# Kernel tuning notes

Hardware: AMD Instinct MI355X
Metric: run time of the kernel (lower is better)

Reference implementation:

```python
import jax, jax.numpy as jnp
import numpy as np

# ---- fixed architecture constants (hard-coded in Wavenet_Barebones.__init__) ----
B = 2
T_FRAMES = 64
UPS = (4, 4, 4, 4)
T = T_FRAMES * 256            # 16384 audio samples
VOCAB = 259
CH = 128
CC = 80                       # conditioning (mel) channels
K = 3                         # dilated conv kernel size
LAYERS = 24
LAYERS_PER_STACK = 6          # 24 // 4
FC1 = 512


def setup_inputs() -> dict:
    key = jax.random.key(0)
    ks = iter(jax.random.split(key, 32))
    nrm = lambda shape, s: jax.random.normal(next(ks), shape, jnp.float32) * s
    return {
        "x": jax.random.randint(next(ks), (B, T), 0, VOCAB),          # mu-law token ids
        "c": jax.random.normal(next(ks), (B, CC, T_FRAMES), jnp.float32),  # mel frames (B,C,Tf)
        "emb": nrm((VOCAB, CH), 1.0),
        "enc_w": nrm((CH, CH), 0.08), "enc_b": jnp.zeros((CH,), jnp.float32),
        "conv_w": nrm((LAYERS, CH, CH, K), 0.05),  # (L, out, in, k)
        "conv_b": jnp.zeros((LAYERS, CH), jnp.float32),
        "cond_w": nrm((LAYERS, CH, CC), 0.05),     # per-layer 1x1 local-conditioning proj
        "cond_b": jnp.zeros((LAYERS, CH), jnp.float32),
        "fc1_w": nrm((FC1, CH), 0.08), "fc1_b": jnp.zeros((FC1,), jnp.float32),
        "fc2_w": nrm((VOCAB, FC1), 0.04), "fc2_b": jnp.zeros((VOCAB,), jnp.float32),
        "ups_w": nrm((4, 3, 4), 0.3),              # 4 ConvTranspose2d kernels (freq=3, time=4)
        "ups_b": jnp.zeros((4,), jnp.float32),
    }


def _upsample(c, ups_w, ups_b):
    """r9y9 UpsampleNetwork: stack of ConvTranspose2d(1,1,(3,s),stride=(1,s),padding=(1,0)) + ReLU.
    c: (B, CC, Tf) -> (B, CC, Tf*256)."""
    y = c[:, None]  # (B, 1, CC, Tf)
    for i, s in enumerate(UPS):
        # transposed conv == input dilation by s + correlation with spatially-flipped kernel
        w = ups_w[i][::-1, ::-1][None, None]  # (O=1, I=1, 3, s)
        y = jax.lax.conv_general_dilated(
            y, w, window_strides=(1, 1),
            padding=[(1, 1), (s - 1, s - 1)],   # freq: kh-1-pad=1; time: kw-1-0=s-1
            lhs_dilation=(1, s),
            dimension_numbers=("NCHW", "OIHW", "NCHW"))
        y = jax.nn.relu(y + ups_b[i])
    return y[:, 0]  # (B, CC, T)


def reference(x, c, emb, enc_w, enc_b, conv_w, conv_b, cond_w, cond_b,
              fc1_w, fc1_b, fc2_w, fc2_b, ups_w, ups_b):
    # encode: embedding -> relu(linear)   (dropout is inference-disabled)
    h = jax.nn.relu(jnp.einsum("btc,oc->bto", emb[x], enc_w) + enc_b)  # (B,T,CH)
    cu = _upsample(c, ups_w, ups_b)                                     # (B,CC,T)
    h = h.transpose(0, 2, 1)                                            # (B,CH,T)
    dn = ("NCH", "OIH", "NCH")
    for l in range(LAYERS):
        d = 2 ** (l % LAYERS_PER_STACK)
        p = (K - 1) * d  # causal left pad
        y = jax.lax.conv_general_dilated(
            h, conv_w[l], window_strides=(1,), padding=[(p, 0)],
            rhs_dilation=(d,), dimension_numbers=dn)
        y = jax.nn.relu(y + conv_b[l][:, None])
        cond = jnp.einsum("oc,bct->bot", cond_w[l], cu) + cond_b[l][:, None]
        h = jax.nn.relu(y + cond + h)  # conditioning + residual, outer F.relu from forward loop
    h = h.transpose(0, 2, 1)                                            # (B,T,CH)
    h = jax.nn.relu(jnp.einsum("btc,oc->bto", h, fc1_w) + fc1_b)
    out = jnp.einsum("btf,of->bto", h, fc2_w) + fc2_b                   # (B,T,VOCAB)
    return out[:, :-1, :]
```

## Files before the change

### kernel.cpp

```cpp
#include <hip/hip_runtime.h>

typedef __bf16 bf16;
typedef __attribute__((ext_vector_type(8))) __bf16 bf16x8;
typedef __attribute__((ext_vector_type(4))) __bf16 bf16x4;
typedef __attribute__((ext_vector_type(4))) float f32x4;

namespace {
constexpr int Bn = 2;
constexpr int T  = 16384;
constexpr int NL = 24;
constexpr int VOC = 259;
}

#define MFMA_B16(a, b, c) __builtin_amdgcn_mfma_f32_16x16x32_bf16((a), (b), (c), 0, 0, 0)

__global__ void prep_wconv_k(const float* __restrict__ cw, const float* __restrict__ dw,
                             bf16* __restrict__ W2) {
  int total = NL * 61440;
  for (int idx = blockIdx.x * 256 + threadIdx.x; idx < total; idx += gridDim.x * 256) {
    int l = idx / 61440; int r = idx % 61440;
    int s = r >> 12; int of = (r >> 9) & 7; int lane = (r >> 3) & 63; int j = r & 7;
    int o = of * 16 + (lane & 15);
    int kk = (lane >> 4) * 8 + j;
    float v;
    if (s < 12) { int k = s >> 2; int c = (s & 3) * 32 + kk; v = cw[((l * 128 + o) * 128 + c) * 3 + k]; }
    else        { int cc = (s - 12) * 32 + kk; v = (cc < 80) ? dw[(l * 128 + o) * 80 + cc] : 0.f; }
    W2[idx] = (bf16)v;
  }
}

__global__ void prep_misc_k(const float* __restrict__ fc1w, const float* __restrict__ encw,
                            const float* __restrict__ emb, const float* __restrict__ fc2w,
                            bf16* __restrict__ fc1wb, bf16* __restrict__ encwb,
                            bf16* __restrict__ embb, bf16* __restrict__ w2f) {
  const int n1 = 65536, n2 = 16384, n3 = 33152, n4 = 196608;
  int total = n1 + n2 + n3 + n4;
  for (int idx = blockIdx.x * 256 + threadIdx.x; idx < total; idx += gridDim.x * 256) {
    if (idx < n1) { fc1wb[idx] = (bf16)fc1w[idx]; }
    else if (idx < n1 + n2) { int i = idx - n1; encwb[i] = (bf16)encw[i]; }
    else if (idx < n1 + n2 + n3) { int i = idx - n1 - n2; embb[i] = (bf16)emb[i]; }
    else {
      int r = idx - n1 - n2 - n3;
      int s = r / 12288; int r2 = r % 12288;
      int ot = r2 >> 9; int lane = (r2 >> 3) & 63; int j = r2 & 7;
      int o = ot * 16 + (lane & 15);
      int f = s * 32 + (lane >> 4) * 8 + j;
      w2f[r] = (bf16)((o < VOC) ? fc2w[o * 512 + f] : 0.f);
    }
  }
}

__global__ void ups_stage_k(const float* __restrict__ in, float* __restrict__ out,
                            const float* __restrict__ W, const float* __restrict__ bptr, int Win) {
  int Wout = Win * 4;
  int total = Bn * 80 * Wout;
  float bias = *bptr;
  for (int idx = blockIdx.x * 256 + threadIdx.x; idx < total; idx += gridDim.x * 256) {
    int w = idx % Wout; int rest = idx / Wout;
    int hrow = rest % 80; int b = rest / 80;
    int win = w >> 2; int kw = w & 3;
    float acc = bias;
#pragma unroll
    for (int kh = 0; kh < 3; ++kh) {
      int hr = hrow + 1 - kh;
      if (hr >= 0 && hr < 80) acc += in[(b * 80 + hr) * Win + win] * W[kh * 4 + kw];
    }
    out[idx] = fmaxf(acc, 0.f);
  }
}

__global__ void ups4_cuT_k(const float* __restrict__ in, const float* __restrict__ W,
                           const float* __restrict__ bptr, bf16* __restrict__ cuT2) {
  int total = Bn * 1024 * 3 * 512;
  float bias = *bptr;
  for (int idx = blockIdx.x * 256 + threadIdx.x; idx < total; idx += gridDim.x * 256) {
    int low = idx & 511; int j = low & 7; int lane = low >> 3;
    int g = idx >> 9; int sc = g % 3; int gt = g / 3; int tile = gt & 1023; int b = gt >> 10;
    int lr = lane & 15, lk = lane >> 4;
    int t = tile * 16 + lr;
    int cc = sc * 32 + lk * 8 + j;
    float v = 0.f;
    if (cc < 80) {
      int win = t >> 2, kw = t & 3;
      float acc = bias;
#pragma unroll
      for (int kh = 0; kh < 3; ++kh) {
        int hr = cc + 1 - kh;
        if (hr >= 0 && hr < 80) acc += in[(b * 80 + hr) * 4096 + win] * W[kh * 4 + kw];
      }
      v = fmaxf(acc, 0.f);
    }
    cuT2[idx] = (bf16)v;
  }
}

__global__ __launch_bounds__(256, 2) void encode_k(
    const int* __restrict__ x, const bf16* __restrict__ embb, const bf16* __restrict__ encwb,
    const float* __restrict__ encb, bf16* __restrict__ hbt) {
  __shared__ char Eb[16384];
  int t0 = blockIdx.x * 64, b = blockIdx.y;
  int tid = threadIdx.x, lane = tid & 63, wid = tid >> 6, wr = wid >> 1, wc = wid & 1;
  int lr = lane & 15, lk = lane >> 4;
  int tb = t0 + wc * 32;
  int xi[2];
#pragma unroll
  for (int n = 0; n < 2; ++n) xi[n] = x[b * T + tb + n * 16 + lr];
  f32x4 acc[4][2] = {};
#pragma unroll
  for (int s = 0; s < 4; ++s) {
    bf16x8 a[4], bb[2];
#pragma unroll
    for (int m = 0; m < 4; ++m) a[m] = *(const bf16x8*)(encwb + (wr * 64 + m * 16 + lr) * 128 + s * 32 + lk * 8);
#pragma unroll
    for (int n = 0; n < 2; ++n) bb[n] = *(const bf16x8*)(embb + xi[n] * 128 + s * 32 + lk * 8);
#pragma unroll
    for (int m = 0; m < 4; ++m)
#pragma unroll
      for (int n = 0; n < 2; ++n) acc[m][n] = MFMA_B16(a[m], bb[n], acc[m][n]);
  }
#pragma unroll
  for (int m = 0; m < 4; ++m)
#pragma unroll
    for (int n = 0; n < 2; ++n) {
      int obase = wr * 64 + m * 16 + lk * 4;
      int row = wc * 32 + n * 16 + lr;
      bf16x4 p;
#pragma unroll
      for (int r = 0; r < 4; ++r) p[r] = (bf16)fmaxf(acc[m][n][r] + encb[obase + r], 0.f);
      int byteo = obase * 2;
      int slot = ((byteo >> 4) ^ (row & 7)) & 15;
      *(bf16x4*)(Eb + row * 256 + (slot << 4) + (byteo & 15)) = p;
    }
  __syncthreads();
  const size_t btb = (size_t)b * T;
  for (int u = tid; u < 1024; u += 256) {
    int row = u >> 4, slot = u & 15;
    uint4 v = *(const uint4*)(Eb + row * 256 + ((((slot) ^ (row & 7)) & 15) << 4));
    *(uint4*)(hbt + (btb + t0 + row) * 128 + slot * 8) = v;
  }
}

template <int D1>
__global__ __launch_bounds__(512, 4) void layer2_k(
    const bf16* __restrict__ hbt_in, bf16* __restrict__ hbt_out,
    const bf16* __restrict__ W2, const bf16* __restrict__ cuT2,
    const float* __restrict__ cb1, const float* __restrict__ db1,
    const float* __restrict__ cb2, const float* __restrict__ db2) {
  constexpr int D2 = 2 * D1;
  constexpr int EXT = (D1 == 16) ? 64 : 16;
  constexpr int NMF = EXT / 16;
  constexpr int NF = NMF + 4;
  constexpr int NCH = (D1 == 16) ? 2 : 1;
  constexpr int NFC = NF / NCH;
  constexpr int AOFF = EXT + 2 * D1;
  constexpr int AR = 64 + AOFF;
  constexpr int BR = 64 + EXT;
  __shared__ uint4 Au[AR * 16];
  __shared__ uint4 Bu[BR * 16];
  char* AB = (char*)Au;
  char* BB = (char*)Bu;
  const int bx = blockIdx.x;
  const int tblk = ((bx & 7) << 5) | (bx >> 3);
  const int t0 = tblk * 64, b = blockIdx.y;
  const int tid = threadIdx.x, lane = tid & 63, wid = tid >> 6;
  const int lr = lane & 15, lk = lane >> 4;
  const size_t btb = (size_t)b * T;
  const size_t bt16 = (size_t)b * 1024;
  const bf16* Wa = W2;
  const bf16* Wb = W2 + 61440;

  uint4 zv; zv.x = zv.y = zv.z = zv.w = 0;
  for (int u = tid; u < AR * 16; u += 512) {
    int row = u >> 4, slot = u & 15;
    int t = t0 - AOFF + row;
    uint4 v = (t >= 0) ? *(const uint4*)(hbt_in + (btb + t) * 128 + slot * 8) : zv;
    *(uint4*)(AB + row * 256 + (((slot ^ (row & 7)) & 15) << 4)) = v;
  }
  __syncthreads();

  f32x4 hl[4];
  const int ob = wid * 16 + lk * 4;
  const f32x4 dv1 = *(const f32x4*)(db1 + ob);
  const int byteo = ob * 2, slot0 = byteo >> 4, wib = byteo & 15;
#pragma unroll
  for (int ch = 0; ch < NCH; ++ch) {
    const int fb = ch * NFC;
    f32x4 acc[NFC] = {};
#pragma unroll
    for (int s = 0; s < 12; ++s) {
      const int k = s >> 2, shift = (k - 2) * D1, sb = (s & 3) * 4;
      bf16x8 a = *(const bf16x8*)(Wa + ((s * 8 + wid) * 64 + lane) * 8);
#pragma unroll
      for (int n = 0; n < NFC; ++n) {
        int row = 2 * D1 + (fb + n) * 16 + lr + shift;
        int slot = ((sb + lk) ^ (row & 7)) & 15;
        bf16x8 bb = *(const bf16x8*)(AB + row * 256 + slot * 16);
        acc[n] = MFMA_B16(a, bb, acc[n]);
      }
    }
    {
      const f32x4 bv = *(const f32x4*)(cb1 + wid * 16 + lk * 4);
#pragma unroll
      for (int n = 0; n < NFC; ++n)
#pragma unroll
        for (int r = 0; r < 4; ++r) acc[n][r] = fmaxf(acc[n][r] + bv[r], 0.f);
    }
#pragma unroll
    for (int s = 12; s < 15; ++s) {
      bf16x8 a = *(const bf16x8*)(Wa + ((s * 8 + wid) * 64 + lane) * 8);
#pragma unroll
      for (int n = 0; n < NFC; ++n) {
        int tb2 = t0 - EXT + (fb + n) * 16;
        int tile = (tb2 < 0 ? 0 : tb2) >> 4;
        bf16x8 bb = *(const bf16x8*)(cuT2 + ((bt16 + tile) * 3 + (s - 12)) * 512 + lane * 8);
        acc[n] = MFMA_B16(a, bb, acc[n]);
      }
    }
#pragma unroll
    for (int n = 0; n < NFC; ++n) {
      const int gn = fb + n;
      const int t = t0 - EXT + gn * 16 + lr;
      const int rowA = 2 * D1 + gn * 16 + lr;
      const int slotA = (slot0 ^ (rowA & 7)) & 15;
      bf16x4 hb = *(const bf16x4*)(AB + rowA * 256 + (slotA << 4) + wib);
      bf16x4 p;
#pragma unroll
      for (int r = 0; r < 4; ++r) {
        float vv = fmaxf(acc[n][r] + dv1[r] + (float)hb[r], 0.f);
        if (t < 0) vv = 0.f;
        if (gn >= NMF) hl[gn - NMF][r] = vv;
        p[r] = (bf16)vv;
      }
      const int rb = gn * 16 + lr;
      *(bf16x4*)(BB + rb * 256 + (((slot0 ^ (rb & 7)) & 15) << 4) + wib) = p;
    }
  }
  __syncthreads();

  f32x4 a2[4] = {};
#pragma unroll
  for (int s = 0; s < 12; ++s) {
    const int k = s >> 2, shift = (k - 2) * D2, sb = (s & 3) * 4;
    bf16x8 a = *(const bf16x8*)(Wb + ((s * 8 + wid) * 64 + lane) * 8);
#pragma unroll
    for (int n = 0; n < 4; ++n) {
      int row = EXT + n * 16 + lr + shift;
      int slot = ((sb + lk) ^ (row & 7)) & 15;
      bf16x8 bb = *(const bf16x8*)(BB + row * 256 + slot * 16);
      a2[n] = MFMA_B16(a, bb, a2[n]);
    }
  }
  {
    const f32x4 bv = *(const f32x4*)(cb2 + wid * 16 + lk * 4);
#pragma unroll
    for (int n = 0; n < 4; ++n)
#pragma unroll
      for (int r = 0; r < 4; ++r) a2[n][r] = fmaxf(a2[n][r] + bv[r], 0.f);
  }
#pragma unroll
  for (int s = 12; s < 15; ++s) {
    bf16x8 a = *(const bf16x8*)(Wb + ((s * 8 + wid) * 64 + lane) * 8);
#pragma unroll
    for (int n = 0; n < 4; ++n) {
      int tile = (t0 + n * 16) >> 4;
      bf16x8 bb = *(const bf16x8*)(cuT2 + ((bt16 + tile) * 3 + (s - 12)) * 512 + lane * 8);
      a2[n] = MFMA_B16(a, bb, a2[n]);
    }
  }
  const f32x4 dv2 = *(const f32x4*)(db2 + ob);
#pragma unroll
  for (int n = 0; n < 4; ++n) {
    bf16x4 p;
#pragma unroll
    for (int r = 0; r < 4; ++r)
      p[r] = (bf16)fmaxf(a2[n][r] + dv2[r] + hl[n][r], 0.f);
    const int rb = n * 16 + lr;
    *(bf16x4*)(AB + rb * 256 + (((slot0 ^ (rb & 7)) & 15) << 4) + wib) = p;
  }
  __syncthreads();
  for (int u = tid; u < 1024; u += 512) {
    int row = u >> 4, slot = u & 15;
    uint4 v = *(const uint4*)(AB + row * 256 + (((slot ^ (row & 7)) & 15) << 4));
    *(uint4*)(hbt_out + (btb + t0 + row) * 128 + slot * 8) = v;
  }
}

__global__ __launch_bounds__(512, 4) void fc1_k(
    const bf16* __restrict__ hbt, const bf16* __restrict__ fc1wb,
    const float* __restrict__ b1, bf16* __restrict__ a1f) {
  __shared__ char H[16384];
  int t0 = blockIdx.x * 64, b = blockIdx.y;
  int tid = threadIdx.x, lane = tid & 63, wid = tid >> 6;
  int lr = lane & 15, lk = lane >> 4;
  const size_t btb = (size_t)b * T;
  for (int u = tid; u < 1024; u += 512) {
    int row = u >> 4, slot = u & 15;
    uint4 v = *(const uint4*)(hbt + (btb + t0 + row) * 128 + slot * 8);
    *(uint4*)(H + row * 256 + (((slot ^ (row & 7)) & 15) << 4)) = v;
  }
  __syncthreads();
  int wf = wid >> 1, wc = wid & 1;
#pragma unroll
  for (int f0 = 0; f0 < 2; ++f0) {
    f32x4 acc[4][2] = {};
#pragma unroll
    for (int s = 0; s < 4; ++s) {
      bf16x8 a[4], bb[2];
#pragma unroll
      for (int m = 0; m < 4; ++m)
        a[m] = *(const bf16x8*)(fc1wb + (f0 * 256 + wf * 64 + m * 16 + lr) * 128 + s * 32 + lk * 8);
#pragma unroll
      for (int n = 0; n < 2; ++n) {
        int row = wc * 32 + n * 16 + lr;
        int slot = ((s * 4 + lk) ^ (row & 7)) & 15;
        bb[n] = *(const bf16x8*)(H + row * 256 + slot * 16);
      }
#pragma unroll
      for (int m = 0; m < 4; ++m)
#pragma unroll
        for (int n = 0; n < 2; ++n) acc[m][n] = MFMA_B16(a[m], bb[n], acc[m][n]);
    }
#pragma unroll
    for (int m = 0; m < 4; ++m) {
      int fb = f0 * 256 + wf * 64 + m * 16 + lk * 4;
      const f32x4 bv = *(const f32x4*)(b1 + fb);
      int lhi = (fb >> 3) & 3, j0 = fb & 7, s16 = fb >> 5;
#pragma unroll
      for (int n = 0; n < 2; ++n) {
        int t = t0 + wc * 32 + n * 16 + lr;
        bf16x4 p;
#pragma unroll
        for (int r = 0; r < 4; ++r) p[r] = (bf16)fmaxf(acc[m][n][r] + bv[r], 0.f);
        size_t addr = (((size_t)b * 1024 + (t >> 4)) * 16 + s16) * 512 + (lhi * 16 + (t & 15)) * 8 + j0;
        *(bf16x4*)(a1f + addr) = p;
      }
    }
  }
}

__global__ __launch_bounds__(512, 4) void fc2_k(
    const bf16* __restrict__ a1f, const bf16* __restrict__ w2f,
    const float* __restrict__ b2, float* __restrict__ out) {
  int t0 = blockIdx.x * 64, b = blockIdx.y;
  int tid = threadIdx.x, lane = tid & 63, wid = tid >> 6;
  int lr = lane & 15, lk = lane >> 4;
  const size_t tb16 = (size_t)b * 1024 + (t0 >> 4);
  f32x4 acc[4][3] = {};
#pragma unroll 4
  for (int s = 0; s < 16; ++s) {
    bf16x8 a[4], bb[3];
#pragma unroll
    for (int mt = 0; mt < 4; ++mt)
      a[mt] = *(const bf16x8*)(a1f + ((tb16 + mt) * 16 + s) * 512 + lane * 8);
#pragma unroll
    for (int no = 0; no < 3; ++no)
      bb[no] = *(const bf16x8*)(w2f + ((s * 24 + wid * 3 + no) * 64 + lane) * 8);
#pragma unroll
    for (int mt = 0; mt < 4; ++mt)
#pragma unroll
      for (int no = 0; no < 3; ++no) acc[mt][no] = MFMA_B16(a[mt], bb[no], acc[mt][no]);
  }
#pragma unroll
  for (int mt = 0; mt < 4; ++mt)
#pragma unroll
    for (int no = 0; no < 3; ++no) {
      int o = (wid * 3 + no) * 16 + lr;
      if (o >= VOC) continue;
      float bias = b2[o];
#pragma unroll
      for (int r = 0; r < 4; ++r) {
        int tg = t0 + mt * 16 + lk * 4 + r;
        if (tg < T - 1) out[((size_t)b * (T - 1) + tg) * VOC + o] = acc[mt][no][r] + bias;
      }
    }
}

extern "C" void kernel_launch(void* const* d_in, const int* in_sizes, int n_in,
                              void* d_out, int out_size, void* d_ws, size_t ws_size,
                              hipStream_t stream) {
  const int*   x      = (const int*)d_in[0];
  const float* c      = (const float*)d_in[1];
  const float* emb    = (const float*)d_in[2];
  const float* enc_w  = (const float*)d_in[3];
  const float* enc_b  = (const float*)d_in[4];
  const float* conv_w = (const float*)d_in[5];
  const float* conv_b = (const float*)d_in[6];
  const float* cond_w = (const float*)d_in[7];
  const float* cond_b = (const float*)d_in[8];
  const float* fc1_w  = (const float*)d_in[9];
  const float* fc1_b  = (const float*)d_in[10];
  const float* fc2_w  = (const float*)d_in[11];
  const float* fc2_b  = (const float*)d_in[12];
  const float* ups_w  = (const float*)d_in[13];
  const float* ups_b  = (const float*)d_in[14];
  float* out = (float*)d_out;
  (void)in_sizes; (void)n_in; (void)out_size; (void)ws_size;

  char* w = (char*)d_ws;
  bf16* hbtA  = (bf16*)w;  w += 8388608;
  bf16* hbtB  = (bf16*)w;  w += 8388608;
  bf16* cuT2  = (bf16*)w;  w += 6291456;
  bf16* W2    = (bf16*)w;  w += 2949120;
  bf16* fc1wb = (bf16*)w;  w += 131072;
  bf16* encwb = (bf16*)w;  w += 32768;
  bf16* embb  = (bf16*)w;  w += 66560;
  bf16* w2f   = (bf16*)w;  w += 393216;
  bf16* a1f   = (bf16*)w;  w += 33554432;
  float* u1   = (float*)w; w += 2621440;
  float* u2   = (float*)w; w += 655360;

  prep_wconv_k<<<dim3(2880), dim3(256), 0, stream>>>(conv_w, cond_w, W2);
  prep_misc_k<<<dim3(1218), dim3(256), 0, stream>>>(fc1_w, enc_w, emb, fc2_w, fc1wb, encwb, embb, w2f);

  ups_stage_k<<<dim3(160),  dim3(256), 0, stream>>>(c,  u1, ups_w + 0,  ups_b + 0, 64);
  ups_stage_k<<<dim3(640),  dim3(256), 0, stream>>>(u1, u2, ups_w + 12, ups_b + 1, 256);
  ups_stage_k<<<dim3(2560), dim3(256), 0, stream>>>(u2, u1, ups_w + 24, ups_b + 2, 1024);
  ups4_cuT_k<<<dim3(4096),  dim3(256), 0, stream>>>(u1, ups_w + 36, ups_b + 3, cuT2);

  encode_k<<<dim3(T / 64, Bn), dim3(256), 0, stream>>>(x, embb, encwb, enc_b, hbtA);

  bf16* hti = hbtA; bf16* hto = hbtB;
  for (int p = 0; p < 12; ++p) {
    int d1 = 1 << ((2 * p) % 6);
    const bf16* wl = W2 + (size_t)p * 2 * 61440;
    const float* cb1 = conv_b + (2 * p) * 128;
    const float* db1 = cond_b + (2 * p) * 128;
    const float* cb2 = conv_b + (2 * p + 1) * 128;
    const float* db2 = cond_b + (2 * p + 1) * 128;
    dim3 g(T / 64, Bn);
    switch (d1) {
      case 1:  layer2_k<1><<<g,  dim3(512), 0, stream>>>(hti, hto, wl, cuT2, cb1, db1, cb2, db2); break;
      case 4:  layer2_k<4><<<g,  dim3(512), 0, stream>>>(hti, hto, wl, cuT2, cb1, db1, cb2, db2); break;
      case 16: layer2_k<16><<<g, dim3(512), 0, stream>>>(hti, hto, wl, cuT2, cb1, db1, cb2, db2); break;
    }
    bf16* t1 = hti; hti = hto; hto = t1;
  }

  fc1_k<<<dim3(T / 64, Bn), dim3(512), 0, stream>>>(hti, fc1wb, fc1_b, a1f);
  fc2_k<<<dim3(T / 64, Bn), dim3(512), 0, stream>>>(a1f, w2f, fc2_b, out);
}
```

Before: 297.5 us.

## Split layer-pair kernel across 16 waves with interleaved row-group work

The fused two-layer kernel goes from 512 to 1024 threads per block. Each wave now handles one 16-channel output slice for half of the time tiles, with the two row groups interleaved, so per-wave accumulator and register use drops. The point is more waves in flight per block to hide LDS and MFMA latency. In exchange, every wave reloads the same weight fragments, the tile-index mapping gets more complex, and the launch bound of 1024 with 4 blocks may limit registers or cap occupancy.

```diff
diff --git a/kernel.cpp b/kernel.cpp
--- a/kernel.cpp
+++ b/kernel.cpp
@@ -141,7 +141,7 @@
 }
 
 template <int D1>
-__global__ __launch_bounds__(512, 4) void layer2_k(
+__global__ __launch_bounds__(1024, 4) void layer2_k(
     const bf16* __restrict__ hbt_in, bf16* __restrict__ hbt_out,
     const bf16* __restrict__ W2, const bf16* __restrict__ cuT2,
     const float* __restrict__ cb1, const float* __restrict__ db1,
@@ -149,9 +149,9 @@
   constexpr int D2 = 2 * D1;
   constexpr int EXT = (D1 == 16) ? 64 : 16;
   constexpr int NMF = EXT / 16;
-  constexpr int NF = NMF + 4;
+  constexpr int NGMAX = (NMF + 1) / 2 + 2;
   constexpr int NCH = (D1 == 16) ? 2 : 1;
-  constexpr int NFC = NF / NCH;
+  constexpr int NGC = NGMAX / NCH;
   constexpr int AOFF = EXT + 2 * D1;
   constexpr int AR = 64 + AOFF;
   constexpr int BR = 64 + EXT;
@@ -163,14 +163,16 @@
   const int tblk = ((bx & 7) << 5) | (bx >> 3);
   const int t0 = tblk * 64, b = blockIdx.y;
   const int tid = threadIdx.x, lane = tid & 63, wid = tid >> 6;
+  const int o = wid & 7, rg = wid >> 3;
   const int lr = lane & 15, lk = lane >> 4;
   const size_t btb = (size_t)b * T;
   const size_t bt16 = (size_t)b * 1024;
   const bf16* Wa = W2;
   const bf16* Wb = W2 + 61440;
+  const int n0 = (NMF + rg) & 1;
 
   uint4 zv; zv.x = zv.y = zv.z = zv.w = 0;
-  for (int u = tid; u < AR * 16; u += 512) {
+  for (int u = tid; u < AR * 16; u += 1024) {
     int row = u >> 4, slot = u & 15;
     int t = t0 - AOFF + row;
     uint4 v = (t >= 0) ? *(const uint4*)(hbt_in + (btb + t) * 128 + slot * 8) : zv;
@@ -178,108 +180,116 @@
   }
   __syncthreads();
 
-  f32x4 hl[4];
-  const int ob = wid * 16 + lk * 4;
+  f32x4 hl[2];
+  const int ob = o * 16 + lk * 4;
   const f32x4 dv1 = *(const f32x4*)(db1 + ob);
+  const f32x4 cv1 = *(const f32x4*)(cb1 + ob);
   const int byteo = ob * 2, slot0 = byteo >> 4, wib = byteo & 15;
 #pragma unroll
   for (int ch = 0; ch < NCH; ++ch) {
-    const int fb = ch * NFC;
-    f32x4 acc[NFC] = {};
+    f32x4 acc[NGC] = {};
 #pragma unroll
     for (int s = 0; s < 12; ++s) {
       const int k = s >> 2, shift = (k - 2) * D1, sb = (s & 3) * 4;
-      bf16x8 a = *(const bf16x8*)(Wa + ((s * 8 + wid) * 64 + lane) * 8);
-#pragma unroll
-      for (int n = 0; n < NFC; ++n) {
-        int row = 2 * D1 + (fb + n) * 16 + lr + shift;
-        int slot = ((sb + lk) ^ (row & 7)) & 15;
-        bf16x8 bb = *(const bf16x8*)(AB + row * 256 + slot * 16);
-        acc[n] = MFMA_B16(a, bb, acc[n]);
-      }
-    }
-    {
-      const f32x4 bv = *(const f32x4*)(cb1 + wid * 16 + lk * 4);
-#pragma unroll
-      for (int n = 0; n < NFC; ++n)
-#pragma unroll
-        for (int r = 0; r < 4; ++r) acc[n][r] = fmaxf(acc[n][r] + bv[r], 0.f);
-    }
+      bf16x8 a = *(const bf16x8*)(Wa + ((s * 8 + o) * 64 + lane) * 8);
+#pragma unroll
+      for (int gi = 0; gi < NGC; ++gi) {
+        const int gidx = ch * NGC + gi;
+        const int gn = (gidx < 2) ? (NMF + n0 + 2 * gidx) : (rg + 2 * (gidx - 2));
+        if (gidx < 2 || rg + 2 * (gidx - 2) < NMF) {
+          int row = 2 * D1 + gn * 16 + lr + shift;
+          int slot = ((sb + lk) ^ (row & 7)) & 15;
+          bf16x8 bb = *(const bf16x8*)(AB + row * 256 + slot * 16);
+          acc[gi] = MFMA_B16(a, bb, acc[gi]);
+        }
+      }
+    }
+#pragma unroll
+    for (int gi = 0; gi < NGC; ++gi)
+#pragma unroll
+      for (int r = 0; r < 4; ++r) acc[gi][r] = fmaxf(acc[gi][r] + cv1[r], 0.f);
 #pragma unroll
     for (int s = 12; s < 15; ++s) {
-      bf16x8 a = *(const bf16x8*)(Wa + ((s * 8 + wid) * 64 + lane) * 8);
-#pragma unroll
-      for (int n = 0; n < NFC; ++n) {
-        int tb2 = t0 - EXT + (fb + n) * 16;
-        int tile = (tb2 < 0 ? 0 : tb2) >> 4;
-        bf16x8 bb = *(const bf16x8*)(cuT2 + ((bt16 + tile) * 3 + (s - 12)) * 512 + lane * 8);
-        acc[n] = MFMA_B16(a, bb, acc[n]);
-      }
-    }
-#pragma unroll
-    for (int n = 0; n < NFC; ++n) {
-      const int gn = fb + n;
-      const int t = t0 - EXT + gn * 16 + lr;
-      const int rowA = 2 * D1 + gn * 16 + lr;
-      const int slotA = (slot0 ^ (rowA & 7)) & 15;
-      bf16x4 hb = *(const bf16x4*)(AB + rowA * 256 + (slotA << 4) + wib);
-      bf16x4 p;
-#pragma unroll
-      for (int r = 0; r < 4; ++r) {
-        float vv = fmaxf(acc[n][r] + dv1[r] + (float)hb[r], 0.f);
-        if (t < 0) vv = 0.f;
-        if (gn >= NMF) hl[gn - NMF][r] = vv;
-        p[r] = (bf16)vv;
-      }
-      const int rb = gn * 16 + lr;
-      *(bf16x4*)(BB + rb * 256 + (((slot0 ^ (rb & 7)) & 15) << 4) + wib) = p;
+      bf16x8 a = *(const bf16x8*)(Wa + ((s * 8 + o) * 64 + lane) * 8);
+#pragma unroll
+      for (int gi = 0; gi < NGC; ++gi) {
+        const int gidx = ch * NGC + gi;
+        const int gn = (gidx < 2) ? (NMF + n0 + 2 * gidx) : (rg + 2 * (gidx - 2));
+        if (gidx < 2 || rg + 2 * (gidx - 2) < NMF) {
+          int tb2 = t0 - EXT + gn * 16;
+          int tile = (tb2 < 0 ? 0 : tb2) >> 4;
+          bf16x8 bb = *(const bf16x8*)(cuT2 + ((bt16 + tile) * 3 + (s - 12)) * 512 + lane * 8);
+          acc[gi] = MFMA_B16(a, bb, acc[gi]);
+        }
+      }
+    }
+#pragma unroll
+    for (int gi = 0; gi < NGC; ++gi) {
+      const int gidx = ch * NGC + gi;
+      const int gn = (gidx < 2) ? (NMF + n0 + 2 * gidx) : (rg + 2 * (gidx - 2));
+      if (gidx < 2 || rg + 2 * (gidx - 2) < NMF) {
+        const int t = t0 - EXT + gn * 16 + lr;
+        const int rowA = 2 * D1 + gn * 16 + lr;
+        const int slotA = (slot0 ^ (rowA & 7)) & 15;
+        bf16x4 hb = *(const bf16x4*)(AB + rowA * 256 + (slotA << 4) + wib);
+        bf16x4 p;
+#pragma unroll
+        for (int r = 0; r < 4; ++r) {
+          float vv = fmaxf(acc[gi][r] + dv1[r] + (float)hb[r], 0.f);
+          if (gidx >= 2 && t < 0) vv = 0.f;
+          if (gidx < 2) hl[gidx][r] = vv;
+          p[r] = (bf16)vv;
+        }
+        const int rb = gn * 16 + lr;
+        *(bf16x4*)(BB + rb * 256 + (((slot0 ^ (rb & 7)) & 15) << 4) + wib) = p;
+      }
     }
   }
   __syncthreads();
 
-  f32x4 a2[4] = {};
+  f32x4 a2[2] = {};
 #pragma unroll
   for (int s = 0; s < 12; ++s) {
     const int k = s >> 2, shift = (k - 2) * D2, sb = (s & 3) * 4;
-    bf16x8 a = *(const bf16x8*)(Wb + ((s * 8 + wid) * 64 + lane) * 8);
-#pragma unroll
-    for (int n = 0; n < 4; ++n) {
-      int row = EXT + n * 16 + lr + shift;
+    bf16x8 a = *(const bf16x8*)(Wb + ((s * 8 + o) * 64 + lane) * 8);
+#pragma unroll
+    for (int mi = 0; mi < 2; ++mi) {
+      int row = EXT + (n0 + 2 * mi) * 16 + lr + shift;
       int slot = ((sb + lk) ^ (row & 7)) & 15;
       bf16x8 bb = *(const bf16x8*)(BB + row * 256 + slot * 16);
-      a2[n] = MFMA_B16(a, bb, a2[n]);
+      a2[mi] = MFMA_B16(a, bb, a2[mi]);
     }
   }
   {
-    const f32x4 bv = *(const f32x4*)(cb2 + wid * 16 + lk * 4);
-#pragma unroll
-    for (int n = 0; n < 4; ++n)
-#pragma unroll
-      for (int r = 0; r < 4; ++r) a2[n][r] = fmaxf(a2[n][r] + bv[r], 0.f);
+    const f32x4 bv = *(const f32x4*)(cb2 + ob);
+#pragma unroll
+    for (int mi = 0; mi < 2; ++mi)
+#pragma unroll
+      for (int r = 0; r < 4; ++r) a2[mi][r] = fmaxf(a2[mi][r] + bv[r], 0.f);
   }
 #pragma unroll
   for (int s = 12; s < 15; ++s) {
-    bf16x8 a = *(const bf16x8*)(Wb + ((s * 8 + wid) * 64 + lane) * 8);
-#pragma unroll
-    for (int n = 0; n < 4; ++n) {
-      int tile = (t0 + n * 16) >> 4;
+    bf16x8 a = *(const bf16x8*)(Wb + ((s * 8 + o) * 64 + lane) * 8);
+#pragma unroll
+    for (int mi = 0; mi < 2; ++mi) {
+      int tile = (t0 + (n0 + 2 * mi) * 16) >> 4;
       bf16x8 bb = *(const bf16x8*)(cuT2 + ((bt16 + tile) * 3 + (s - 12)) * 512 + lane * 8);
-      a2[n] = MFMA_B16(a, bb, a2[n]);
+      a2[mi] = MFMA_B16(a, bb, a2[mi]);
     }
   }
   const f32x4 dv2 = *(const f32x4*)(db2 + ob);
 #pragma unroll
-  for (int n = 0; n < 4; ++n) {
+  for (int mi = 0; mi < 2; ++mi) {
     bf16x4 p;
 #pragma unroll
     for (int r = 0; r < 4; ++r)
-      p[r] = (bf16)fmaxf(a2[n][r] + dv2[r] + hl[n][r], 0.f);
-    const int rb = n * 16 + lr;
+      p[r] = (bf16)fmaxf(a2[mi][r] + dv2[r] + hl[mi][r], 0.f);
+    const int rb = (n0 + 2 * mi) * 16 + lr;
     *(bf16x4*)(AB + rb * 256 + (((slot0 ^ (rb & 7)) & 15) << 4) + wib) = p;
   }
   __syncthreads();
-  for (int u = tid; u < 1024; u += 512) {
-    int row = u >> 4, slot = u & 15;
+  {
+    int row = tid >> 4, slot = tid & 15;
     uint4 v = *(const uint4*)(AB + row * 256 + (((slot ^ (row & 7)) & 15) << 4));
     *(uint4*)(hbt_out + (btb + t0 + row) * 128 + slot * 8) = v;
   }
@@ -429,9 +439,9 @@
     const float* db2 = cond_b + (2 * p + 1) * 128;
     dim3 g(T / 64, Bn);
     switch (d1) {
-      case 1:  layer2_k<1><<<g,  dim3(512), 0, stream>>>(hti, hto, wl, cuT2, cb1, db1, cb2, db2); break;
-      case 4:  layer2_k<4><<<g,  dim3(512), 0, stream>>>(hti, hto, wl, cuT2, cb1, db1, cb2, db2); break;
-      case 16: layer2_k<16><<<g, dim3(512), 0, stream>>>(hti, hto, wl, cuT2, cb1, db1, cb2, db2); break;
+      case 1:  layer2_k<1><<<g,  dim3(1024), 0, stream>>>(hti, hto, wl, cuT2, cb1, db1, cb2, db2); break;
+      case 4:  layer2_k<4><<<g,  dim3(1024), 0, stream>>>(hti, hto, wl, cuT2, cb1, db1, cb2, db2); break;
+      case 16: layer2_k<16><<<g, dim3(1024), 0, stream>>>(hti, hto, wl, cuT2, cb1, db1, cb2, db2); break;
     }
     bf16* t1 = hti; hti = hto; hto = t1;
   }
```

Result: slower. 332.6 us (+11.8%).

## Fuse four dilated layers (d=1,2,4,8) per stack into one kernel with halo recompute

Applied to the files above, without the earlier changes.

Adds a layer4_k kernel that loads a 64-row causal halo plus the 64-row tile into shared memory and runs four dilated conv+conditioning layers back to back. Each layer shrinks the valid extent, so intermediates stay in LDS. The host loop now launches one layer4_k and one layer2_k<16> per stack, replacing three layer2_k launches. This cuts launches and global round trips of the hidden state, at the cost of redundant halo computation and more LDS per block, which may reduce occupancy.

```diff
diff --git a/kernel.cpp b/kernel.cpp
--- a/kernel.cpp
+++ b/kernel.cpp
@@ -137,6 +137,114 @@
     int row = u >> 4, slot = u & 15;
     uint4 v = *(const uint4*)(Eb + row * 256 + ((((slot) ^ (row & 7)) & 15) << 4));
     *(uint4*)(hbt + (btb + t0 + row) * 128 + slot * 8) = v;
+  }
+}
+
+template <int D, int NF, int ESRC, int EDST>
+__device__ __forceinline__ void qlayer(
+    const char* __restrict__ SRC, char* __restrict__ DST,
+    const bf16* __restrict__ W, const bf16* __restrict__ cuT2,
+    size_t bt16, int t0, const float* __restrict__ cb, const float* __restrict__ dbv,
+    int wid, int lane, int lr, int lk) {
+  constexpr int NCH = (NF > 5) ? 2 : 1;
+  constexpr int NC0 = (NF + NCH - 1) / NCH;
+  const int ob = wid * 16 + lk * 4;
+  const f32x4 cv = *(const f32x4*)(cb + ob);
+  const f32x4 dv = *(const f32x4*)(dbv + ob);
+  const int byteo = ob * 2, slot0 = byteo >> 4, wib = byteo & 15;
+#pragma unroll
+  for (int ch = 0; ch < NCH; ++ch) {
+    const int fb = ch * NC0;
+    f32x4 acc[NC0] = {};
+#pragma unroll
+    for (int s = 0; s < 12; ++s) {
+      const int k = s >> 2, shift = (k - 2) * D, sb = (s & 3) * 4;
+      bf16x8 a = *(const bf16x8*)(W + ((s * 8 + wid) * 64 + lane) * 8);
+#pragma unroll
+      for (int n = 0; n < NC0; ++n) {
+        if (fb + n < NF) {
+          int row = (fb + n) * 16 + (ESRC - EDST) + lr + shift;
+          int slot = ((sb + lk) ^ (row & 7)) & 15;
+          bf16x8 bb = *(const bf16x8*)(SRC + row * 256 + slot * 16);
+          acc[n] = MFMA_B16(a, bb, acc[n]);
+        }
+      }
+    }
+#pragma unroll
+    for (int n = 0; n < NC0; ++n)
+#pragma unroll
+      for (int r = 0; r < 4; ++r) acc[n][r] = fmaxf(acc[n][r] + cv[r], 0.f);
+#pragma unroll
+    for (int s = 12; s < 15; ++s) {
+      bf16x8 a = *(const bf16x8*)(W + ((s * 8 + wid) * 64 + lane) * 8);
+#pragma unroll
+      for (int n = 0; n < NC0; ++n) {
+        if (fb + n < NF) {
+          int tb2 = t0 - EDST + (fb + n) * 16;
+          int tile = (tb2 < 0 ? 0 : tb2) >> 4;
+          bf16x8 bb = *(const bf16x8*)(cuT2 + ((bt16 + tile) * 3 + (s - 12)) * 512 + lane * 8);
+          acc[n] = MFMA_B16(a, bb, acc[n]);
+        }
+      }
+    }
+#pragma unroll
+    for (int n = 0; n < NC0; ++n) {
+      if (fb + n < NF) {
+        const int gn = fb + n;
+        const int t = t0 - EDST + gn * 16 + lr;
+        const int rowS = gn * 16 + (ESRC - EDST) + lr;
+        const int slotS = (slot0 ^ (rowS & 7)) & 15;
+        bf16x4 hb = *(const bf16x4*)(SRC + rowS * 256 + (slotS << 4) + wib);
+        const int rb = gn * 16 + lr;
+        bf16x4 p;
+#pragma unroll
+        for (int r = 0; r < 4; ++r) {
+          float vv = fmaxf(acc[n][r] + dv[r] + (float)hb[r], 0.f);
+          if (t < 0) vv = 0.f;
+          p[r] = (bf16)vv;
+        }
+        *(bf16x4*)(DST + rb * 256 + (((slot0 ^ (rb & 7)) & 15) << 4) + wib) = p;
+      }
+    }
+  }
+}
+
+__global__ __launch_bounds__(512, 4) void layer4_k(
+    const bf16* __restrict__ hbt_in, bf16* __restrict__ hbt_out,
+    const bf16* __restrict__ W4, const bf16* __restrict__ cuT2,
+    const float* __restrict__ cb, const float* __restrict__ db) {
+  __shared__ uint4 B0u[128 * 16];
+  __shared__ uint4 B1u[112 * 16];
+  char* B0 = (char*)B0u;
+  char* B1 = (char*)B1u;
+  const int bx = blockIdx.x;
+  const int tblk = ((bx & 7) << 5) | (bx >> 3);
+  const int t0 = tblk * 64, b = blockIdx.y;
+  const int tid = threadIdx.x, lane = tid & 63, wid = tid >> 6;
+  const int lr = lane & 15, lk = lane >> 4;
+  const size_t btb = (size_t)b * T;
+  const size_t bt16 = (size_t)b * 1024;
+
+  uint4 zv; zv.x = zv.y = zv.z = zv.w = 0;
+  for (int u = tid; u < 128 * 16; u += 512) {
+    int row = u >> 4, slot = u & 15;
+    int t = t0 - 64 + row;
+    uint4 v = (t >= 0) ? *(const uint4*)(hbt_in + (btb + t) * 128 + slot * 8) : zv;
+    *(uint4*)(B0 + row * 256 + (((slot ^ (row & 7)) & 15) << 4)) = v;
+  }
+  __syncthreads();
+  qlayer<1, 7, 64, 48>(B0, B1, W4,             cuT2, bt16, t0, cb,       db,       wid, lane, lr, lk);
+  __syncthreads();
+  qlayer<2, 6, 48, 32>(B1, B0, W4 + 61440,     cuT2, bt16, t0, cb + 128, db + 128, wid, lane, lr, lk);
+  __syncthreads();
+  qlayer<4, 5, 32, 16>(B0, B1, W4 + 2 * 61440, cuT2, bt16, t0, cb + 256, db + 256, wid, lane, lr, lk);
+  __syncthreads();
+  qlayer<8, 4, 16, 0>(B1, B0, W4 + 3 * 61440,  cuT2, bt16, t0, cb + 384, db + 384, wid, lane, lr, lk);
+  __syncthreads();
+  for (int u = tid; u < 1024; u += 512) {
+    int row = u >> 4, slot = u & 15;
+    uint4 v = *(const uint4*)(B0 + row * 256 + (((slot ^ (row & 7)) & 15) << 4));
+    *(uint4*)(hbt_out + (btb + t0 + row) * 128 + slot * 8) = v;
   }
 }
 
@@ -420,20 +528,17 @@
   encode_k<<<dim3(T / 64, Bn), dim3(256), 0, stream>>>(x, embb, encwb, enc_b, hbtA);
 
   bf16* hti = hbtA; bf16* hto = hbtB;
-  for (int p = 0; p < 12; ++p) {
-    int d1 = 1 << ((2 * p) % 6);
-    const bf16* wl = W2 + (size_t)p * 2 * 61440;
-    const float* cb1 = conv_b + (2 * p) * 128;
-    const float* db1 = cond_b + (2 * p) * 128;
-    const float* cb2 = conv_b + (2 * p + 1) * 128;
-    const float* db2 = cond_b + (2 * p + 1) * 128;
-    dim3 g(T / 64, Bn);
-    switch (d1) {
-      case 1:  layer2_k<1><<<g,  dim3(512), 0, stream>>>(hti, hto, wl, cuT2, cb1, db1, cb2, db2); break;
-      case 4:  layer2_k<4><<<g,  dim3(512), 0, stream>>>(hti, hto, wl, cuT2, cb1, db1, cb2, db2); break;
-      case 16: layer2_k<16><<<g, dim3(512), 0, stream>>>(hti, hto, wl, cuT2, cb1, db1, cb2, db2); break;
-    }
-    bf16* t1 = hti; hti = hto; hto = t1;
+  dim3 g(T / 64, Bn);
+  for (int st = 0; st < 4; ++st) {
+    int l0 = st * 6;
+    layer4_k<<<g, dim3(512), 0, stream>>>(hti, hto, W2 + (size_t)l0 * 61440, cuT2,
+                                          conv_b + l0 * 128, cond_b + l0 * 128);
+    { bf16* t1 = hti; hti = hto; hto = t1; }
+    int lp = l0 + 4;
+    layer2_k<16><<<g, dim3(512), 0, stream>>>(hti, hto, W2 + (size_t)lp * 61440, cuT2,
+                                              conv_b + lp * 128, cond_b + lp * 128,
+                                              conv_b + (lp + 1) * 128, cond_b + (lp + 1) * 128);
+    { bf16* t1 = hti; hti = hto; hto = t1; }
   }
 
   fc1_k<<<dim3(T / 64, Bn), dim3(512), 0, stream>>>(hti, fc1wb, fc1_b, a1f);
```

Measured after the change: 276.7 us (median of 2 runs). -7.0%, faster.
